# Optimization experiments

Measured on AMD Instinct MI355X. Metric: run time of the kernel, lower is better.

Reference implementation:

```python
import jax, jax.numpy as jnp
import numpy as np

DIM = 512
HEADS = 8
DIM_HEAD = 64
ROT_DIM = DIM_HEAD // 2  # RotaryEmbedding(dim_head // 2)
B = 4
N = 8192


def rotate_every_two(x):
    # '... (d j) -> ... d j', j=2 ; (x1, x2) -> (-x2, x1) interleaved back
    x1 = x[..., 0::2]
    x2 = x[..., 1::2]
    return jnp.stack((-x2, x1), axis=-1).reshape(x.shape)


def apply_rotary_emb(freqs, t):
    # freqs: [1,1,n,rot_dim]; rotary on first rot_dim channels, passthrough rest
    rot_dim = freqs.shape[-1]
    t_rot, t_pass = t[..., :rot_dim], t[..., rot_dim:]
    t_rot = t_rot * jnp.cos(freqs) + rotate_every_two(t_rot) * jnp.sin(freqs)
    return jnp.concatenate((t_rot, t_pass), axis=-1)


def rotary_freqs(n):
    # lucidrains RotaryEmbedding(ROT_DIM): inv_freq over ROT_DIM//2, repeated r=2
    inv_freq = 1.0 / (10000.0 ** (jnp.arange(0, ROT_DIM, 2, dtype=jnp.float32) / ROT_DIM))
    f = jnp.arange(n, dtype=jnp.float32)[:, None] * inv_freq[None, :]  # [n, ROT_DIM//2]
    return jnp.repeat(f, 2, axis=-1)  # [n, ROT_DIM]


def setup_inputs() -> dict:
    key = jax.random.key(0)
    ks = jax.random.split(key, 8)
    inner = HEADS * DIM_HEAD
    s = lambda fan_in: 1.0 / np.sqrt(fan_in)
    return {
        "x": jax.random.normal(ks[0], (B, N, DIM), dtype=jnp.float32),
        "w_qkv": jax.random.uniform(ks[1], (DIM, inner * 3), jnp.float32, -s(DIM), s(DIM)),
        "w_q_logits": jax.random.uniform(ks[2], (DIM_HEAD, 1), jnp.float32, -s(DIM_HEAD), s(DIM_HEAD)),
        "w_k_logits": jax.random.uniform(ks[3], (DIM_HEAD // 2, 1), jnp.float32, -s(DIM_HEAD // 2), s(DIM_HEAD // 2)),
        "w_r": jax.random.uniform(ks[4], (DIM_HEAD // 2, DIM_HEAD), jnp.float32, -s(DIM_HEAD // 2), s(DIM_HEAD // 2)),
        "b_r": jax.random.uniform(ks[5], (DIM_HEAD,), jnp.float32, -s(DIM_HEAD // 2), s(DIM_HEAD // 2)),
        "w_out": jax.random.uniform(ks[6], (inner, DIM), jnp.float32, -s(inner), s(inner)),
        "b_out": jax.random.uniform(ks[7], (DIM,), jnp.float32, -s(inner), s(inner)),
    }


def reference(x, w_qkv, w_q_logits, w_k_logits, w_r, b_r, w_out, b_out):
    b, n, _ = x.shape
    h, d = HEADS, DIM_HEAD
    scale = d ** -0.5

    qkv = x @ w_qkv  # [b,n,3*h*d]
    q, k, v = jnp.split(qkv, 3, axis=-1)
    to_bhnd = lambda t: t.reshape(b, n, h, d).transpose(0, 2, 1, 3)
    q, k, v = to_bhnd(q), to_bhnd(k), to_bhnd(v)

    freqs = rotary_freqs(n)[None, None]  # [1,1,n,ROT_DIM]
    q_aggr = apply_rotary_emb(freqs, q)
    k_aggr = apply_rotary_emb(freqs, k)
    v_aggr = v

    q_attn = jax.nn.softmax((q @ w_q_logits)[..., 0] * scale, axis=-1)  # [b,h,n]
    global_q = jnp.einsum('bhn,bhnd->bhd', q_attn, q_aggr)[:, :, None]  # [b,h,1,d]

    kk = (k * global_q).reshape(b, h, n, d // 2, 2).sum(-1)  # sum adjacent pairs -> [b,h,n,d/2]
    k_attn = jax.nn.softmax((kk @ w_k_logits)[..., 0] * scale, axis=-1)
    global_k = jnp.einsum('bhn,bhnd->bhd', k_attn, k_aggr)[:, :, None]  # [b,h,1,d]

    u = (v_aggr * global_k).reshape(b, h, n, d // 2, 2).sum(-1)  # [b,h,n,d/2]
    r = u @ w_r + b_r  # [b,h,n,d]
    r = r + q
    r = r.transpose(0, 2, 1, 3).reshape(b, n, h * d)
    return r @ w_out + b_out
```

## Files before the change

kernel.cpp:

```cpp
#include <hip/hip_runtime.h>
#include <hip/hip_bf16.h>

typedef __attribute__((ext_vector_type(8))) short s16x8;
typedef __attribute__((ext_vector_type(4))) short s16x4;
typedef __attribute__((ext_vector_type(4))) float f32x4;

#define SEQ 8192

__device__ __forceinline__ float bf2f(short s){
  union { unsigned u; float f; } c; c.u = ((unsigned)(unsigned short)s) << 16; return c.f;
}
__device__ __forceinline__ short f2bf(float f){
  __hip_bfloat16 h = __float2bfloat16(f);
  short s; __builtin_memcpy(&s, &h, 2); return s;
}

__device__ __forceinline__ void transpose_body(const float* __restrict__ in, __hip_bfloat16* __restrict__ out,
                                               int R, int C, int bx, int by){
  __shared__ float tile[32][33];
  int c0 = bx*32, r0 = by*32;
  int tx = threadIdx.x & 31, ty = threadIdx.x >> 5;
  #pragma unroll
  for (int i = ty; i < 32; i += 8) tile[i][tx] = in[(size_t)(r0+i)*C + c0 + tx];
  __syncthreads();
  #pragma unroll
  for (int i = ty; i < 32; i += 8) out[(size_t)(c0+i)*R + r0 + tx] = __float2bfloat16(tile[tx][i]);
}

__global__ __launch_bounds__(256) void prep(
    const float* __restrict__ x, __hip_bfloat16* __restrict__ xb, unsigned* __restrict__ tab,
    const float* __restrict__ wqkv, __hip_bfloat16* __restrict__ wqkvT,
    const float* __restrict__ wout, __hip_bfloat16* __restrict__ woutT)
{
  int b = blockIdx.x;
  if (b < 16384){
    int i = b*256 + threadIdx.x;
    float4 v = reinterpret_cast<const float4*>(x)[i];
    s16x4 o = { f2bf(v.x), f2bf(v.y), f2bf(v.z), f2bf(v.w) };
    reinterpret_cast<s16x4*>(xb)[i] = o;
  } else if (b < 18432){
    int idx = (b - 16384)*256 + threadIdx.x;
    int n = idx >> 6, d = idx & 63;
    float c, s;
    if (d < 32){
      float ex = -(float)(d & ~1) / 32.0f;
      float invf = __expf(ex * 9.210340371976184f);
      float f = (float)n * invf;
      c = cosf(f);
      s = sinf(f);
      s = (d & 1) ? s : -s;
    } else { c = 1.f; s = 0.f; }
    tab[idx] = (unsigned)(unsigned short)f2bf(c) | ((unsigned)(unsigned short)f2bf(s) << 16);
  } else if (b < 19200){
    int id = b - 18432;
    transpose_body(wqkv, wqkvT, 512, 1536, id % 48, id / 48);
  } else {
    int id = b - 19200;
    transpose_body(wout, woutT, 512, 512, id % 16, id / 16);
  }
}

template<int MODE>
__global__ __launch_bounds__(512, 4) void gemm128(
    const __hip_bfloat16* __restrict__ A, const __hip_bfloat16* __restrict__ BT,
    int M, int Nn, int K,
    __hip_bfloat16* __restrict__ oQ, __hip_bfloat16* __restrict__ oK, __hip_bfloat16* __restrict__ oV,
    float* __restrict__ oF, const float* __restrict__ bias)
{
  __shared__ __align__(16) char lds[73728];
  const int t = threadIdx.x;
  const int lane = t & 63, wid = t >> 6;
  const int lr = lane & 15, lg = lane >> 4;
  const int wm   = (wid >> 2) * 64;
  const int wn64 = (wid & 3) * 64;

  int nwg = gridDim.x, per = nwg >> 3, wg = blockIdx.x;
  int swz = (wg & 7) * per + (wg >> 3);
  int nblk = Nn >> 8;
  int bm = (swz / nblk) << 7;
  int bn = (swz % nblk) << 8;

  const int NKT = K >> 5;

  const __hip_bfloat16* spp[3];
  int dofs[3];
  #pragma unroll
  for (int i = 0; i < 3; ++i){
    int g = (i == 0) ? t : (t + (i-1)*512);
    int row = g >> 2, ch = g & 3;
    int sch = ch ^ ((row >> 1) & 3);
    spp[i] = (i == 0 ? A + (size_t)(bm + row)*K : BT + (size_t)(bn + row)*K) + sch*8;
    dofs[i] = ((i == 0) ? 0 : 8192) + g*16;
  }
  #define STG(i, kt2, bufo) __builtin_amdgcn_global_load_lds( \
      (const __attribute__((address_space(1))) void*)(spp[i] + (size_t)(kt2)*32), \
      (__attribute__((address_space(3))) void*)(lds + (bufo) + dofs[i]), 16, 0, 0)

  STG(0, 0, 0); STG(1, 0, 0); STG(2, 0, 0);
  STG(0, 1, 24576); STG(1, 1, 24576); STG(2, 1, 24576);

  f32x4 acc[4][4] = {};
  int rOff = 0, sOff = 49152;
  #define SWR(r) ((((r) >> 1) & 3) << 4)

  for (int kt = 0; kt < NKT; ++kt){
    if (kt + 1 < NKT) asm volatile("s_waitcnt vmcnt(3)" ::: "memory");
    else              asm volatile("s_waitcnt vmcnt(0)" ::: "memory");
    __builtin_amdgcn_s_barrier();
    __builtin_amdgcn_sched_barrier(0);
    if (kt + 2 < NKT){ STG(0, kt+2, sOff); STG(1, kt+2, sOff); STG(2, kt+2, sOff); }
    const char* lb = lds + rOff;
    s16x8 af[4], bfr[4];
    #pragma unroll
    for (int f = 0; f < 4; ++f){
      int r = wm + f*16 + lr;
      af[f] = *reinterpret_cast<const s16x8*>(lb + (r << 6) + ((lg << 4) ^ SWR(r)));
    }
    #pragma unroll
    for (int f = 0; f < 4; ++f){
      int r = wn64 + f*16 + lr;
      bfr[f] = *reinterpret_cast<const s16x8*>(lb + 8192 + (r << 6) + ((lg << 4) ^ SWR(r)));
    }
    __builtin_amdgcn_s_setprio(1);
    #pragma unroll
    for (int mi = 0; mi < 4; ++mi)
      #pragma unroll
      for (int ni = 0; ni < 4; ++ni)
        acc[mi][ni] = __builtin_amdgcn_mfma_f32_16x16x32_bf16(bfr[ni], af[mi], acc[mi][ni], 0, 0, 0);
    __builtin_amdgcn_s_setprio(0);
    rOff = (rOff == 49152) ? 0 : rOff + 24576;
    sOff = (sOff == 49152) ? 0 : sOff + 24576;
  }
  __builtin_amdgcn_s_barrier();

  if (MODE == 0){
    char* reg = lds + wid*8192;
    #pragma unroll
    for (int mi = 0; mi < 4; ++mi){
      #pragma unroll
      for (int ni = 0; ni < 4; ++ni){
        int tok = mi*16 + lr;
        int sl = (ni*4 + lg) ^ (tok & 15);
        ushort4 w4;
        w4.x = (unsigned short)f2bf(acc[mi][ni][0]);
        w4.y = (unsigned short)f2bf(acc[mi][ni][1]);
        w4.z = (unsigned short)f2bf(acc[mi][ni][2]);
        w4.w = (unsigned short)f2bf(acc[mi][ni][3]);
        *reinterpret_cast<unsigned long long*>(reg + tok*128 + sl*8) =
            *reinterpret_cast<unsigned long long*>(&w4);
      }
    }
    asm volatile("s_waitcnt lgkmcnt(0)" ::: "memory");
    __builtin_amdgcn_sched_barrier(0);
    int gcol = bn + wn64;
    int ts = gcol >> 9, rem = gcol & 511, h = rem >> 6;
    __hip_bfloat16* dstT = (ts == 0) ? oQ : ((ts == 1) ? oK : oV);
    int tokbase = bm + wm;
    int bb = tokbase >> 13;
    dstT += ((size_t)(bb*8 + h)) << 19;
    #pragma unroll
    for (int p2 = 0; p2 < 8; ++p2){
      int tok = p2*8 + (lane >> 3);
      int l0 = (lane & 7) * 2;
      unsigned long long u0 = *reinterpret_cast<const unsigned long long*>(reg + tok*128 + ((l0 ^ (tok & 15)))*8);
      unsigned long long u1 = *reinterpret_cast<const unsigned long long*>(reg + tok*128 + (((l0+1) ^ (tok & 15)))*8);
      int n = (tokbase + tok) & 8191;
      unsigned long long o2[2] = { u0, u1 };
      *reinterpret_cast<s16x8*>(dstT + ((size_t)n << 6) + (lane & 7)*8) =
          *reinterpret_cast<const s16x8*>(o2);
    }
  } else {
    #pragma unroll
    for (int mi = 0; mi < 4; ++mi){
      #pragma unroll
      for (int ni = 0; ni < 4; ++ni){
        int gc = bn + wn64 + ni*16 + lg*4;
        int gr = bm + wm + mi*16 + lr;
        float4 bv = *reinterpret_cast<const float4*>(bias + gc);
        float4 o;
        o.x = acc[mi][ni][0] + bv.x;
        o.y = acc[mi][ni][1] + bv.y;
        o.z = acc[mi][ni][2] + bv.z;
        o.w = acc[mi][ni][3] + bv.w;
        *reinterpret_cast<float4*>(oF + (size_t)gr*Nn + gc) = o;
      }
    }
  }
  #undef STG
  #undef SWR
}

template<int SRC>
__global__ __launch_bounds__(256) void fused_stats(
    const __hip_bfloat16* __restrict__ T, const float* __restrict__ svec,
    const float* __restrict__ partsIn, const float* __restrict__ wkl,
    const unsigned* __restrict__ tab, float* __restrict__ outp)
{
  int chunk = blockIdx.x, bh = blockIdx.y;
  int t = threadIdx.x, lane = t & 63, w = t >> 6;
  __shared__ float sv[64];
  __shared__ float ev[256];
  __shared__ float redv[4][64];
  __shared__ float rede[4];
  if (t < 64){
    float s;
    if (SRC == 0){
      s = svec[t] * 0.125f;
    } else {
      const float* pp = partsIn;
      float tot = 0.f, g = 0.f;
      #pragma unroll 4
      for (int i = 0; i < 32; ++i){ tot += pp[i*66 + 1]; g += pp[i*66 + 2 + t]; }
      s = (g / tot) * wkl[t >> 1] * 0.125f;
    }
    sv[t] = s;
  }
  __syncthreads();

  int n = chunk*256 + t;
  const __hip_bfloat16* row = T + ((size_t)bh*SEQ + n)*64;
  float s = 0.f;
  #pragma unroll
  for (int dv = 0; dv < 8; ++dv){
    s16x8 v8 = *reinterpret_cast<const s16x8*>(row + dv*8);
    #pragma unroll
    for (int e = 0; e < 8; ++e) s += bf2f(v8[e]) * sv[dv*8 + e];
  }
  ev[t] = __expf(s);
  __syncthreads();

  const short* Tsh = reinterpret_cast<const short*>(T + ((size_t)bh*SEQ)*64);
  float acc = 0.f, se = 0.f;
  int nb = chunk*256 + w*64;
  #pragma unroll 4
  for (int i = 0; i < 64; ++i){
    int n2 = nb + i;
    float e = ev[w*64 + i];
    float xv = bf2f(Tsh[(size_t)n2*64 + lane]);
    float xo = __shfl_xor(xv, 1, 64);
    unsigned cs = tab[n2*64 + lane];
    float c  = bf2f((short)(cs & 0xffff));
    float s2 = bf2f((short)(cs >> 16));
    acc += e * (xv*c + xo*s2);
    se += e;
  }
  redv[w][lane] = acc;
  if (lane == 0) rede[w] = se;
  __syncthreads();
  if (t < 64){
    float* ob = outp + (size_t)(bh*32 + chunk)*66;
    ob[2 + t] = redv[0][t] + redv[1][t] + redv[2][t] + redv[3][t];
    if (t == 0) ob[1] = rede[0] + rede[1] + rede[2] + rede[3];
  }
}

__global__ __launch_bounds__(256) void epilogue_r(
    const __hip_bfloat16* __restrict__ vT, const __hip_bfloat16* __restrict__ qT,
    const float* __restrict__ partsK, const float* __restrict__ wr, const float* __restrict__ br,
    __hip_bfloat16* __restrict__ rb)
{
  int idx = blockIdx.x*256 + threadIdx.x;
  int bh = idx >> 13, nl = idx & 8191;
  int b = bh >> 3, h = bh & 7;
  int t = threadIdx.x;
  __shared__ float sgk[64];
  if (t < 64){
    const float* pp = partsK + (size_t)bh*32*66;
    float tot = 0.f, g = 0.f;
    #pragma unroll 4
    for (int i = 0; i < 32; ++i){ tot += pp[i*66 + 1]; g += pp[i*66 + 2 + t]; }
    sgk[t] = g / tot;
  }
  __syncthreads();

  const __hip_bfloat16* vrow = vT + (size_t)idx*64;
  const __hip_bfloat16* qrow = qT + (size_t)idx*64;
  float u[32];
  #pragma unroll
  for (int dv = 0; dv < 8; ++dv){
    s16x8 v8 = *reinterpret_cast<const s16x8*>(vrow + dv*8);
    #pragma unroll
    for (int e = 0; e < 8; e += 2){
      int d = dv*8 + e;
      u[d >> 1] = bf2f(v8[e])*sgk[d] + bf2f(v8[e+1])*sgk[d+1];
    }
  }
  __hip_bfloat16* rrow = rb + ((size_t)(b*SEQ + nl))*512 + h*64;
  #pragma unroll 2
  for (int dv = 0; dv < 8; ++dv){
    s16x8 q8 = *reinterpret_cast<const s16x8*>(qrow + dv*8);
    s16x8 o8;
    #pragma unroll
    for (int e = 0; e < 8; ++e){
      int d = dv*8 + e;
      float a2 = br[d] + bf2f(q8[e]);
      #pragma unroll
      for (int j = 0; j < 32; ++j) a2 += u[j] * wr[j*64 + d];
      o8[e] = f2bf(a2);
    }
    *reinterpret_cast<s16x8*>(rrow + dv*8) = o8;
  }
}

extern "C" void kernel_launch(void* const* d_in, const int* in_sizes, int n_in,
                              void* d_out, int out_size, void* d_ws, size_t ws_size,
                              hipStream_t stream)
{
  (void)in_sizes; (void)n_in; (void)out_size; (void)ws_size;
  const float* x    = (const float*)d_in[0];
  const float* wqkv = (const float*)d_in[1];
  const float* wql  = (const float*)d_in[2];
  const float* wkl  = (const float*)d_in[3];
  const float* wr   = (const float*)d_in[4];
  const float* br   = (const float*)d_in[5];
  const float* wout = (const float*)d_in[6];
  const float* bout = (const float*)d_in[7];
  float* out = (float*)d_out;

  char* p = (char*)d_ws;
  auto alloc = [&](size_t bytes){ char* r = p; p += (bytes + 255) & ~(size_t)255; return r; };
  __hip_bfloat16* xb    = (__hip_bfloat16*)alloc(33554432);
  __hip_bfloat16* wqkvT = (__hip_bfloat16*)alloc(1572864);
  __hip_bfloat16* woutT = (__hip_bfloat16*)alloc(524288);
  __hip_bfloat16* qT = (__hip_bfloat16*)alloc(33554432);
  __hip_bfloat16* kT = (__hip_bfloat16*)alloc(33554432);
  __hip_bfloat16* vT = (__hip_bfloat16*)alloc(33554432);
  __hip_bfloat16* rb = (__hip_bfloat16*)alloc(33554432);
  unsigned* tab = (unsigned*)alloc(2097152);

  float* partsQ = (float*)xb;
  float* partsK = partsQ + 32*32*66;

  prep<<<19456, 256, 0, stream>>>(x, xb, tab, wqkv, wqkvT, wout, woutT);

  gemm128<0><<<1536, 512, 0, stream>>>(xb, wqkvT, 32768, 1536, 512,
                                       qT, kT, vT, nullptr, nullptr);

  fused_stats<0><<<dim3(32,32), 256, 0, stream>>>(qT, wql, nullptr, nullptr, tab, partsQ);
  fused_stats<1><<<dim3(32,32), 256, 0, stream>>>(kT, nullptr, partsQ, wkl, tab, partsK);

  epilogue_r<<<1024, 256, 0, stream>>>(vT, qT, partsK, wr, br, rb);

  gemm128<1><<<512, 512, 0, stream>>>(rb, woutT, 32768, 512, 512,
                                      nullptr, nullptr, nullptr, out, bout);
}
```

Measured before the change: 192.1 us.

## Enlarge GEMM tiles to 256x256 with phased 8-wave ping-pong pipeline

```diff
diff --git a/kernel.cpp b/kernel.cpp
--- a/kernel.cpp
+++ b/kernel.cpp
@@ -61,82 +61,104 @@
 }
 
 template<int MODE>
-__global__ __launch_bounds__(512, 4) void gemm128(
+__global__ __launch_bounds__(512, 2) void gemm8(
     const __hip_bfloat16* __restrict__ A, const __hip_bfloat16* __restrict__ BT,
-    int M, int Nn, int K,
+    int M, int Nn,
     __hip_bfloat16* __restrict__ oQ, __hip_bfloat16* __restrict__ oK, __hip_bfloat16* __restrict__ oV,
     float* __restrict__ oF, const float* __restrict__ bias)
 {
-  __shared__ __align__(16) char lds[73728];
+  constexpr int K = 512, NKT = 8;
+  __shared__ __align__(16) char lds[131072];
   const int t = threadIdx.x;
   const int lane = t & 63, wid = t >> 6;
   const int lr = lane & 15, lg = lane >> 4;
-  const int wm   = (wid >> 2) * 64;
-  const int wn64 = (wid & 3) * 64;
+  const int wm = (wid >> 2) * 128;
+  const int wn = (wid & 3) * 64;
 
   int nwg = gridDim.x, per = nwg >> 3, wg = blockIdx.x;
   int swz = (wg & 7) * per + (wg >> 3);
   int nblk = Nn >> 8;
-  int bm = (swz / nblk) << 7;
+  int bm = (swz / nblk) << 8;
   int bn = (swz % nblk) << 8;
 
-  const int NKT = K >> 5;
-
-  const __hip_bfloat16* spp[3];
-  int dofs[3];
-  #pragma unroll
-  for (int i = 0; i < 3; ++i){
-    int g = (i == 0) ? t : (t + (i-1)*512);
-    int row = g >> 2, ch = g & 3;
-    int sch = ch ^ ((row >> 1) & 3);
-    spp[i] = (i == 0 ? A + (size_t)(bm + row)*K : BT + (size_t)(bn + row)*K) + sch*8;
-    dofs[i] = ((i == 0) ? 0 : 8192) + g*16;
-  }
-  #define STG(i, kt2, bufo) __builtin_amdgcn_global_load_lds( \
-      (const __attribute__((address_space(1))) void*)(spp[i] + (size_t)(kt2)*32), \
-      (__attribute__((address_space(3))) void*)(lds + (bufo) + dofs[i]), 16, 0, 0)
-
-  STG(0, 0, 0); STG(1, 0, 0); STG(2, 0, 0);
-  STG(0, 1, 24576); STG(1, 1, 24576); STG(2, 1, 24576);
-
-  f32x4 acc[4][4] = {};
-  int rOff = 0, sOff = 49152;
-  #define SWR(r) ((((r) >> 1) & 3) << 4)
-
+  const __hip_bfloat16* pA[2]; const __hip_bfloat16* pB[2]; int dof[2];
+  #pragma unroll
+  for (int i = 0; i < 2; ++i){
+    int g = t + i*512;
+    int row = g >> 2, cw = g & 3;
+    int sc = cw ^ ((row >> 1) & 3);
+    pA[i] = A  + (size_t)(bm + row)*K + sc*8;
+    pB[i] = BT + (size_t)(bn + row)*K + sc*8;
+    dof[i] = g * 16;
+  }
+  #define STG_A(kt, kh) do { _Pragma("unroll") for (int i = 0; i < 2; ++i) \
+      __builtin_amdgcn_global_load_lds( \
+        (const __attribute__((address_space(1))) void*)(pA[i] + (kt)*64 + (kh)*32), \
+        (__attribute__((address_space(3))) void*)(lds + (((kt) & 1) << 16) + (kh)*16384 + dof[i]), 16, 0, 0); } while(0)
+  #define STG_B(kt, kh) do { _Pragma("unroll") for (int i = 0; i < 2; ++i) \
+      __builtin_amdgcn_global_load_lds( \
+        (const __attribute__((address_space(1))) void*)(pB[i] + (kt)*64 + (kh)*32), \
+        (__attribute__((address_space(3))) void*)(lds + (((kt) & 1) << 16) + 32768 + (kh)*16384 + dof[i]), 16, 0, 0); } while(0)
+
+  STG_B(0, 0); STG_A(0, 0); STG_B(0, 1); STG_A(0, 1);
+  STG_B(1, 0); STG_A(1, 0); STG_B(1, 1);
+
+  f32x4 acc[8][4] = {};
+  s16x8 af[4], bfr[4];
+
+  #define LDA(mh, kh, kt) do { _Pragma("unroll") for (int f = 0; f < 4; ++f){ \
+      int r = wm + (mh)*64 + f*16 + lr; \
+      af[f] = *reinterpret_cast<const s16x8*>(lds + (((kt) & 1) << 16) + (kh)*16384 + (r << 6) \
+              + (((lg ^ ((r >> 1) & 3)) << 4))); } } while(0)
+  #define LDB(kh, kt) do { _Pragma("unroll") for (int f = 0; f < 4; ++f){ \
+      int r = wn + f*16 + lr; \
+      bfr[f] = *reinterpret_cast<const s16x8*>(lds + (((kt) & 1) << 16) + 32768 + (kh)*16384 + (r << 6) \
+              + (((lg ^ ((r >> 1) & 3)) << 4))); } } while(0)
+  #define PH_MFMA(mh) do { __builtin_amdgcn_s_setprio(1); \
+    _Pragma("unroll") for (int m2 = 0; m2 < 4; ++m2) \
+    _Pragma("unroll") for (int ni = 0; ni < 4; ++ni) \
+      acc[(mh)*4 + m2][ni] = __builtin_amdgcn_mfma_f32_16x16x32_bf16(bfr[ni], af[m2], acc[(mh)*4 + m2][ni], 0, 0, 0); \
+    __builtin_amdgcn_s_setprio(0); } while(0)
+  #define BARS() do { __builtin_amdgcn_s_barrier(); __builtin_amdgcn_sched_barrier(0); } while(0)
+
+  asm volatile("s_waitcnt vmcnt(10)" ::: "memory");
+  BARS();
+
+  #pragma unroll
   for (int kt = 0; kt < NKT; ++kt){
-    if (kt + 1 < NKT) asm volatile("s_waitcnt vmcnt(3)" ::: "memory");
-    else              asm volatile("s_waitcnt vmcnt(0)" ::: "memory");
-    __builtin_amdgcn_s_barrier();
-    __builtin_amdgcn_sched_barrier(0);
-    if (kt + 2 < NKT){ STG(0, kt+2, sOff); STG(1, kt+2, sOff); STG(2, kt+2, sOff); }
-    const char* lb = lds + rOff;
-    s16x8 af[4], bfr[4];
-    #pragma unroll
-    for (int f = 0; f < 4; ++f){
-      int r = wm + f*16 + lr;
-      af[f] = *reinterpret_cast<const s16x8*>(lb + (r << 6) + ((lg << 4) ^ SWR(r)));
-    }
-    #pragma unroll
-    for (int f = 0; f < 4; ++f){
-      int r = wn64 + f*16 + lr;
-      bfr[f] = *reinterpret_cast<const s16x8*>(lb + 8192 + (r << 6) + ((lg << 4) ^ SWR(r)));
-    }
-    __builtin_amdgcn_s_setprio(1);
-    #pragma unroll
-    for (int mi = 0; mi < 4; ++mi)
-      #pragma unroll
-      for (int ni = 0; ni < 4; ++ni)
-        acc[mi][ni] = __builtin_amdgcn_mfma_f32_16x16x32_bf16(bfr[ni], af[mi], acc[mi][ni], 0, 0, 0);
-    __builtin_amdgcn_s_setprio(0);
-    rOff = (rOff == 49152) ? 0 : rOff + 24576;
-    sOff = (sOff == 49152) ? 0 : sOff + 24576;
-  }
-  __builtin_amdgcn_s_barrier();
+    LDA(0, 0, kt); LDB(0, kt);
+    if (kt + 1 < NKT) STG_A(kt+1, 1);
+    BARS();
+    PH_MFMA(0);
+    BARS();
+    LDA(1, 0, kt);
+    if (kt + 2 < NKT) STG_B(kt+2, 0);
+    BARS();
+    PH_MFMA(1);
+    if (kt <= NKT - 3)      asm volatile("s_waitcnt vmcnt(10)" ::: "memory");
+    else if (kt == NKT - 2) asm volatile("s_waitcnt vmcnt(8)"  ::: "memory");
+    else                    asm volatile("s_waitcnt vmcnt(0)"  ::: "memory");
+    BARS();
+    LDA(0, 1, kt); LDB(1, kt);
+    if (kt + 2 < NKT) STG_A(kt+2, 0);
+    BARS();
+    PH_MFMA(0);
+    BARS();
+    LDA(1, 1, kt);
+    if (kt + 2 < NKT) STG_B(kt+2, 1);
+    BARS();
+    PH_MFMA(1);
+    if (kt + 1 < NKT){
+      if (kt <= NKT - 3) asm volatile("s_waitcnt vmcnt(10)" ::: "memory");
+      else               asm volatile("s_waitcnt vmcnt(4)"  ::: "memory");
+    }
+    BARS();
+  }
 
   if (MODE == 0){
-    char* reg = lds + wid*8192;
-    #pragma unroll
-    for (int mi = 0; mi < 4; ++mi){
+    char* reg = lds + wid*16384;
+    #pragma unroll
+    for (int mi = 0; mi < 8; ++mi){
       #pragma unroll
       for (int ni = 0; ni < 4; ++ni){
         int tok = mi*16 + lr;
@@ -152,14 +174,14 @@
     }
     asm volatile("s_waitcnt lgkmcnt(0)" ::: "memory");
     __builtin_amdgcn_sched_barrier(0);
-    int gcol = bn + wn64;
+    int gcol = bn + wn;
     int ts = gcol >> 9, rem = gcol & 511, h = rem >> 6;
     __hip_bfloat16* dstT = (ts == 0) ? oQ : ((ts == 1) ? oK : oV);
     int tokbase = bm + wm;
     int bb = tokbase >> 13;
     dstT += ((size_t)(bb*8 + h)) << 19;
     #pragma unroll
-    for (int p2 = 0; p2 < 8; ++p2){
+    for (int p2 = 0; p2 < 16; ++p2){
       int tok = p2*8 + (lane >> 3);
       int l0 = (lane & 7) * 2;
       unsigned long long u0 = *reinterpret_cast<const unsigned long long*>(reg + tok*128 + ((l0 ^ (tok & 15)))*8);
@@ -171,10 +193,10 @@
     }
   } else {
     #pragma unroll
-    for (int mi = 0; mi < 4; ++mi){
+    for (int mi = 0; mi < 8; ++mi){
       #pragma unroll
       for (int ni = 0; ni < 4; ++ni){
-        int gc = bn + wn64 + ni*16 + lg*4;
+        int gc = bn + wn + ni*16 + lg*4;
         int gr = bm + wm + mi*16 + lr;
         float4 bv = *reinterpret_cast<const float4*>(bias + gc);
         float4 o;
@@ -186,8 +208,12 @@
       }
     }
   }
-  #undef STG
-  #undef SWR
+  #undef STG_A
+  #undef STG_B
+  #undef LDA
+  #undef LDB
+  #undef PH_MFMA
+  #undef BARS
 }
 
 template<int SRC>
@@ -333,14 +359,14 @@
 
   prep<<<19456, 256, 0, stream>>>(x, xb, tab, wqkv, wqkvT, wout, woutT);
 
-  gemm128<0><<<1536, 512, 0, stream>>>(xb, wqkvT, 32768, 1536, 512,
-                                       qT, kT, vT, nullptr, nullptr);
+  gemm8<0><<<768, 512, 0, stream>>>(xb, wqkvT, 32768, 1536,
+                                    qT, kT, vT, nullptr, nullptr);
 
   fused_stats<0><<<dim3(32,32), 256, 0, stream>>>(qT, wql, nullptr, nullptr, tab, partsQ);
   fused_stats<1><<<dim3(32,32), 256, 0, stream>>>(kT, nullptr, partsQ, wkl, tab, partsK);
 
   epilogue_r<<<1024, 256, 0, stream>>>(vT, qT, partsK, wr, br, rb);
 
-  gemm128<1><<<512, 512, 0, stream>>>(rb, woutT, 32768, 512, 512,
-                                      nullptr, nullptr, nullptr, out, bout);
-}
+  gemm8<1><<<256, 512, 0, stream>>>(rb, woutT, 32768, 512,
+                                    nullptr, nullptr, nullptr, out, bout);
+}
```

Result: no change. 192.2 us (+0.0%).
